# Kernel tuning notes

Measured on AMD Instinct MI355X. Metric: run time of the kernel, lower is better.

The kernel has to match this reference:

```python
import jax, jax.numpy as jnp
import numpy as np

LAMBDA = 5.0  # lambda_ init arg


def setup_inputs() -> dict:
    key = jax.random.key(0)
    k1, k2 = jax.random.split(key)
    B, D, K = 131072, 512, 112
    return {
        "x": jax.random.normal(k1, (B, D), dtype=jnp.float32),
        "cluster_centers": jax.random.normal(k2, (K, D), dtype=jnp.float32),
        "topk": 5,
    }


def reference(x, cluster_centers, topk):
    # similarity to all cluster centers: [B, K]
    sims = x @ cluster_centers.T
    # top-k cluster indices per row: [B, k]
    _, idx = jax.lax.top_k(sims, topk)
    # gather selected centers: [B, k, D]
    Ac = cluster_centers[idx]
    # re-score selected centers against the query, softmax over k
    scores = jax.nn.softmax(jnp.einsum('bkd,bd->bk', Ac, x), axis=-1)
    # softmax-weighted aggregation, scaled, plus residual
    Tc = LAMBDA * jnp.einsum('bk,bkd->bd', scores, Ac)
    return Tc + x
```

## Files before the change

kernel.cpp:

```cpp
#include <hip/hip_runtime.h>
#include <math.h>

#define D_DIM 512
#define K_DIM 112
#define TOPK  5
#define LAMBDA_ 5.0f

#define BM 128
#define BK 64
#define TM 8
#define TN 14
#define NTHREADS 128
#define XS_LD 132
#define CT_LD 128
#define NCAND (8 * TOPK)
#define CAND_LD 41

__device__ float g_ct[D_DIM * CT_LD];

__global__ __launch_bounds__(128)
void transpose_c(const float* __restrict__ cc) {
  const int d = blockIdx.x;
  const int k = threadIdx.x;
  if (k < K_DIM)
    g_ct[d * CT_LD + (k / TN) * 16 + (k % TN)] = cc[k * D_DIM + d];
}

struct __align__(16) SMem {
  union {
    float xs[BK * XS_LD];
    struct {
      float         cv[BM][CAND_LD];
      unsigned char ci[BM][CAND_LD];
      float         sc[BM][TOPK];
      int           si[BM][TOPK];
    } p;
  } u;
};

__global__ __launch_bounds__(NTHREADS, 2)
void tse_fused(const float* __restrict__ x, const float* __restrict__ cc,
               float* __restrict__ out) {
  __shared__ SMem sm;
  const int tid = threadIdx.x;
  const int ky  = tid & 7;
  const int tx  = tid >> 3;
  const long long row0 = (long long)blockIdx.x * BM;

  float acc[TM][TN];
#pragma unroll
  for (int i = 0; i < TM; ++i)
#pragma unroll
    for (int j = 0; j < TN; ++j) acc[i][j] = 0.0f;

#pragma unroll 1
  for (int dc = 0; dc < D_DIM; dc += BK) {
#pragma unroll
    for (int it = 0; it < (BM * BK / 4) / NTHREADS; ++it) {
      int t  = it * NTHREADS + tid;
      int dg = t & 15;
      int r  = t >> 4;
      float4 v = *(const float4*)(x + (row0 + r) * D_DIM + dc + dg * 4);
      int d0 = dg * 4;
      int rw = r ^ (((dg >> 1) & 7) << 2);
      sm.u.xs[(d0 + 0) * XS_LD + rw] = v.x;
      sm.u.xs[(d0 + 1) * XS_LD + rw] = v.y;
      sm.u.xs[(d0 + 2) * XS_LD + rw] = v.z;
      sm.u.xs[(d0 + 3) * XS_LD + rw] = v.w;
    }
    __syncthreads();

    const float* ctp = g_ct + dc * CT_LD + ky * 16;
#pragma unroll 4
    for (int dl = 0; dl < BK; ++dl) {
      const int rho = ((dl >> 3) & 7) << 2;
      const float* xrow = &sm.u.xs[dl * XS_LD];
      const int off = (tx * TM) ^ rho;
      float4 xa = *(const float4*)(xrow + off);
      float4 xb = *(const float4*)(xrow + (off ^ 4));
      float xf[TM] = {xa.x, xa.y, xa.z, xa.w, xb.x, xb.y, xb.z, xb.w};
      const float4* cp = (const float4*)(ctp + dl * CT_LD);
      float4 c0 = cp[0], c1 = cp[1], c2 = cp[2], c3 = cp[3];
      float cf[TN] = {c0.x, c0.y, c0.z, c0.w, c1.x, c1.y, c1.z, c1.w,
                      c2.x, c2.y, c2.z, c2.w, c3.x, c3.y};
#pragma unroll
      for (int i = 0; i < TM; ++i)
#pragma unroll
        for (int j = 0; j < TN; ++j)
          acc[i][j] = fmaf(xf[i], cf[j], acc[i][j]);
    }
    __syncthreads();
  }

#pragma unroll
  for (int i = 0; i < TM; ++i) {
    float tv[TOPK]; int ti[TOPK];
#pragma unroll
    for (int s = 0; s < TOPK; ++s) { tv[s] = -3.0e38f; ti[s] = 0; }
#pragma unroll
    for (int j = 0; j < TN; ++j) {
      float v = acc[i][j];
      if (v > tv[TOPK - 1]) {
        tv[TOPK - 1] = v; ti[TOPK - 1] = ky * TN + j;
#pragma unroll
        for (int s = TOPK - 2; s >= 0; --s) {
          if (tv[s + 1] > tv[s]) {
            float tf = tv[s]; tv[s] = tv[s + 1]; tv[s + 1] = tf;
            int   tq = ti[s]; ti[s] = ti[s + 1]; ti[s + 1] = tq;
          }
        }
      }
    }
    int r = tx * TM + i;
#pragma unroll
    for (int s = 0; s < TOPK; ++s) {
      sm.u.p.cv[r][ky * TOPK + s] = tv[s];
      sm.u.p.ci[r][ky * TOPK + s] = (unsigned char)ti[s];
    }
  }
  __syncthreads();

  {
    const int r = tid;
    float tv[TOPK]; int ti[TOPK];
#pragma unroll
    for (int s = 0; s < TOPK; ++s) { tv[s] = -3.0e38f; ti[s] = 0; }
    for (int c = 0; c < NCAND; ++c) {
      float v = sm.u.p.cv[r][c];
      if (v > tv[TOPK - 1]) {
        tv[TOPK - 1] = v; ti[TOPK - 1] = (int)sm.u.p.ci[r][c];
#pragma unroll
        for (int s = TOPK - 2; s >= 0; --s) {
          if (tv[s + 1] > tv[s]) {
            float tf = tv[s]; tv[s] = tv[s + 1]; tv[s + 1] = tf;
            int   tq = ti[s]; ti[s] = ti[s + 1]; ti[s + 1] = tq;
          }
        }
      }
    }
    float m = tv[0];
    float e[TOPK]; float z = 0.0f;
#pragma unroll
    for (int s = 0; s < TOPK; ++s) { e[s] = __expf(tv[s] - m); z += e[s]; }
    float sl = LAMBDA_ / z;
#pragma unroll
    for (int s = 0; s < TOPK; ++s) { sm.u.p.sc[r][s] = e[s] * sl; sm.u.p.si[r][s] = ti[s]; }
  }
  __syncthreads();

  {
    const int dg = tid;
    for (int r = 0; r < BM; ++r) {
      const long long base = (row0 + r) * D_DIM + dg * 4;
      float4 o = *(const float4*)(x + base);
#pragma unroll
      for (int t = 0; t < TOPK; ++t) {
        float w  = sm.u.p.sc[r][t];
        int   ix = sm.u.p.si[r][t];
        const float4 cv = *(const float4*)(cc + (long long)ix * D_DIM + dg * 4);
        o.x = fmaf(w, cv.x, o.x);
        o.y = fmaf(w, cv.y, o.y);
        o.z = fmaf(w, cv.z, o.z);
        o.w = fmaf(w, cv.w, o.w);
      }
      *(float4*)(out + base) = o;
    }
  }
}

extern "C" void kernel_launch(void* const* d_in, const int* in_sizes, int n_in,
                              void* d_out, int out_size, void* d_ws, size_t ws_size,
                              hipStream_t stream) {
  const float* x  = (const float*)d_in[0];
  const float* cc = (const float*)d_in[1];
  float* out = (float*)d_out;
  const int Btot = in_sizes[0] / D_DIM;
  const int grid = Btot / BM;
  transpose_c<<<dim3(D_DIM), dim3(128), 0, stream>>>(cc);
  tse_fused<<<dim3(grid), dim3(NTHREADS), 0, stream>>>(x, cc, out);
}
```

Measured before the change: 807.1 us.

## Restructure similarity GEMM to 4 waves with wave-uniform center slices

Moves from 128 threads with an 8x14 register tile to 256 threads, where each wave owns 28 cluster centers and each lane owns 2 rows. Center values now come from wave-uniform addresses, which can be scalar or broadcast loads, while each lane reads x through a float2 LDS access. The top-k merge drops to 20 candidates and the output phase splits rows over both thread halves. The transposed center buffer moves into the workspace, with a fallback to a device symbol. In exchange, each thread does fewer FMAs per load and the x-loads have less reuse, which may hurt arithmetic intensity.

New measurement: 725.7 us. 1.11x faster.

```diff
diff --git a/kernel.cpp b/kernel.cpp
--- a/kernel.cpp
+++ b/kernel.cpp
@@ -8,22 +8,23 @@
 
 #define BM 128
 #define BK 64
-#define TM 8
-#define TN 14
-#define NTHREADS 128
+#define NTHREADS 256
+#define KPW 28
+#define CT_LD 128
 #define XS_LD 132
-#define CT_LD 128
-#define NCAND (8 * TOPK)
-#define CAND_LD 41
+#define NCAND (4 * TOPK)
+#define CAND_LD 21
 
-__device__ float g_ct[D_DIM * CT_LD];
+#define CT_BYTES (D_DIM * CT_LD * sizeof(float))
+
+static __device__ float g_ct_fallback[D_DIM * CT_LD];
 
 __global__ __launch_bounds__(128)
-void transpose_c(const float* __restrict__ cc) {
+void transpose_c(const float* __restrict__ cc, float* __restrict__ ct) {
   const int d = blockIdx.x;
   const int k = threadIdx.x;
   if (k < K_DIM)
-    g_ct[d * CT_LD + (k / TN) * 16 + (k % TN)] = cc[k * D_DIM + d];
+    ct[d * CT_LD + (k / KPW) * 32 + (k % KPW)] = cc[k * D_DIM + d];
 }
 
 struct __align__(16) SMem {
@@ -31,27 +32,27 @@
     float xs[BK * XS_LD];
     struct {
       float         cv[BM][CAND_LD];
-      unsigned char ci[BM][CAND_LD];
       float         sc[BM][TOPK];
       int           si[BM][TOPK];
+      unsigned char ci[BM][24];
     } p;
   } u;
 };
 
-__global__ __launch_bounds__(NTHREADS, 2)
+__global__ __launch_bounds__(NTHREADS, 4)
 void tse_fused(const float* __restrict__ x, const float* __restrict__ cc,
-               float* __restrict__ out) {
+               const float* __restrict__ ct, float* __restrict__ out) {
   __shared__ SMem sm;
-  const int tid = threadIdx.x;
-  const int ky  = tid & 7;
-  const int tx  = tid >> 3;
+  const int tid  = threadIdx.x;
+  const int lane = tid & 63;
+  const int w = __builtin_amdgcn_readfirstlane(tid >> 6);
   const long long row0 = (long long)blockIdx.x * BM;
 
-  float acc[TM][TN];
+  float acc[2][KPW];
 #pragma unroll
-  for (int i = 0; i < TM; ++i)
+  for (int i = 0; i < 2; ++i)
 #pragma unroll
-    for (int j = 0; j < TN; ++j) acc[i][j] = 0.0f;
+    for (int j = 0; j < KPW; ++j) acc[i][j] = 0.0f;
 
 #pragma unroll 1
   for (int dc = 0; dc < D_DIM; dc += BK) {
@@ -70,38 +71,34 @@
     }
     __syncthreads();
 
-    const float* ctp = g_ct + dc * CT_LD + ky * 16;
+    const float* ctp = ct + (long long)dc * CT_LD + w * 32;
 #pragma unroll 4
     for (int dl = 0; dl < BK; ++dl) {
-      const int rho = ((dl >> 3) & 7) << 2;
-      const float* xrow = &sm.u.xs[dl * XS_LD];
-      const int off = (tx * TM) ^ rho;
-      float4 xa = *(const float4*)(xrow + off);
-      float4 xb = *(const float4*)(xrow + (off ^ 4));
-      float xf[TM] = {xa.x, xa.y, xa.z, xa.w, xb.x, xb.y, xb.z, xb.w};
-      const float4* cp = (const float4*)(ctp + dl * CT_LD);
-      float4 c0 = cp[0], c1 = cp[1], c2 = cp[2], c3 = cp[3];
-      float cf[TN] = {c0.x, c0.y, c0.z, c0.w, c1.x, c1.y, c1.z, c1.w,
-                      c2.x, c2.y, c2.z, c2.w, c3.x, c3.y};
+      const int s = ((dl >> 3) & 7) << 2;
+      const float2 xr = *(const float2*)&sm.u.xs[dl * XS_LD + ((2 * lane) ^ s)];
+      const float* cp = ctp + dl * CT_LD;
+      float cf[KPW];
 #pragma unroll
-      for (int i = 0; i < TM; ++i)
+      for (int j = 0; j < KPW; ++j) cf[j] = cp[j];
 #pragma unroll
-        for (int j = 0; j < TN; ++j)
-          acc[i][j] = fmaf(xf[i], cf[j], acc[i][j]);
+      for (int j = 0; j < KPW; ++j) {
+        acc[0][j] = fmaf(xr.x, cf[j], acc[0][j]);
+        acc[1][j] = fmaf(xr.y, cf[j], acc[1][j]);
+      }
     }
     __syncthreads();
   }
 
 #pragma unroll
-  for (int i = 0; i < TM; ++i) {
+  for (int i = 0; i < 2; ++i) {
     float tv[TOPK]; int ti[TOPK];
 #pragma unroll
     for (int s = 0; s < TOPK; ++s) { tv[s] = -3.0e38f; ti[s] = 0; }
 #pragma unroll
-    for (int j = 0; j < TN; ++j) {
+    for (int j = 0; j < KPW; ++j) {
       float v = acc[i][j];
       if (v > tv[TOPK - 1]) {
-        tv[TOPK - 1] = v; ti[TOPK - 1] = ky * TN + j;
+        tv[TOPK - 1] = v; ti[TOPK - 1] = w * KPW + j;
 #pragma unroll
         for (int s = TOPK - 2; s >= 0; --s) {
           if (tv[s + 1] > tv[s]) {
@@ -111,20 +108,21 @@
         }
       }
     }
-    int r = tx * TM + i;
+    const int r = 2 * lane + i;
 #pragma unroll
     for (int s = 0; s < TOPK; ++s) {
-      sm.u.p.cv[r][ky * TOPK + s] = tv[s];
-      sm.u.p.ci[r][ky * TOPK + s] = (unsigned char)ti[s];
+      sm.u.p.cv[r][w * TOPK + s] = tv[s];
+      sm.u.p.ci[r][w * TOPK + s] = (unsigned char)ti[s];
     }
   }
   __syncthreads();
 
-  {
+  if (tid < BM) {
     const int r = tid;
     float tv[TOPK]; int ti[TOPK];
 #pragma unroll
     for (int s = 0; s < TOPK; ++s) { tv[s] = -3.0e38f; ti[s] = 0; }
+#pragma unroll
     for (int c = 0; c < NCAND; ++c) {
       float v = sm.u.p.cv[r][c];
       if (v > tv[TOPK - 1]) {
@@ -149,19 +147,20 @@
   __syncthreads();
 
   {
-    const int dg = tid;
-    for (int r = 0; r < BM; ++r) {
+    const int dg = tid & 127;
+    int r = tid >> 7;
+    for (; r < BM; r += 2) {
       const long long base = (row0 + r) * D_DIM + dg * 4;
       float4 o = *(const float4*)(x + base);
 #pragma unroll
       for (int t = 0; t < TOPK; ++t) {
-        float w  = sm.u.p.sc[r][t];
+        float w2 = sm.u.p.sc[r][t];
         int   ix = sm.u.p.si[r][t];
         const float4 cv = *(const float4*)(cc + (long long)ix * D_DIM + dg * 4);
-        o.x = fmaf(w, cv.x, o.x);
-        o.y = fmaf(w, cv.y, o.y);
-        o.z = fmaf(w, cv.z, o.z);
-        o.w = fmaf(w, cv.w, o.w);
+        o.x = fmaf(w2, cv.x, o.x);
+        o.y = fmaf(w2, cv.y, o.y);
+        o.z = fmaf(w2, cv.z, o.z);
+        o.w = fmaf(w2, cv.w, o.w);
       }
       *(float4*)(out + base) = o;
     }
@@ -174,8 +173,18 @@
   const float* x  = (const float*)d_in[0];
   const float* cc = (const float*)d_in[1];
   float* out = (float*)d_out;
+
+  float* ct;
+  if (d_ws != nullptr && ws_size >= CT_BYTES) {
+    ct = (float*)d_ws;
+  } else {
+    void* p = nullptr;
+    hipGetSymbolAddress(&p, HIP_SYMBOL(g_ct_fallback));
+    ct = (float*)p;
+  }
+
   const int Btot = in_sizes[0] / D_DIM;
   const int grid = Btot / BM;
-  transpose_c<<<dim3(D_DIM), dim3(128), 0, stream>>>(cc);
-  tse_fused<<<dim3(grid), dim3(NTHREADS), 0, stream>>>(x, cc, out);
+  transpose_c<<<dim3(D_DIM), dim3(128), 0, stream>>>(cc, ct);
+  tse_fused<<<dim3(grid), dim3(NTHREADS), 0, stream>>>(x, cc, ct, out);
 }
```
